# Performance work log

Hardware: AMD Instinct MI355X
Metric: run time of the kernel (lower is better)

The kernel has to match this reference:

```python
import jax, jax.numpy as jnp
import numpy as np

EMBED_DIM = 768
NUM_HEADS = 12
D_K = EMBED_DIM // NUM_HEADS
FFN_DIM = 3072
N_QUBITS = 8
LN_EPS = 1e-5


def layer_norm(x, g, b):
    mu = jnp.mean(x, axis=-1, keepdims=True)
    var = jnp.mean(jnp.square(x - mu), axis=-1, keepdims=True)
    return (x - mu) * jax.lax.rsqrt(var + LN_EPS) * g + b


def setup_inputs() -> dict:
    key = jax.random.key(0)
    ks = jax.random.split(key, 8)
    B, S = 4, 2048
    s_comb = 1.0 / np.sqrt(EMBED_DIM)
    s_w1 = 1.0 / np.sqrt(N_QUBITS)
    s_w2 = 1.0 / np.sqrt(FFN_DIM)
    return {
        "x": jax.random.normal(ks[0], (B, S, EMBED_DIM), jnp.float32),
        "combine_w": jax.random.uniform(ks[1], (EMBED_DIM, EMBED_DIM), jnp.float32, -s_comb, s_comb),
        "theta": jax.random.normal(ks[2], (N_QUBITS,), jnp.float32),
        "w1": jax.random.uniform(ks[3], (FFN_DIM, N_QUBITS), jnp.float32, -s_w1, s_w1),
        "w2": jax.random.uniform(ks[4], (EMBED_DIM, FFN_DIM), jnp.float32, -s_w2, s_w2),
        "ln1_g": jnp.ones((EMBED_DIM,), jnp.float32),
        "ln1_b": jnp.zeros((EMBED_DIM,), jnp.float32),
        "ln2_g": jnp.ones((EMBED_DIM,), jnp.float32),
        "ln2_b": jnp.zeros((EMBED_DIM,), jnp.float32),
    }


def reference(x, combine_w, theta, w1, w2, ln1_g, ln1_b, ln2_g, ln2_b):
    B, S, D = x.shape
    # --- attention (q = k = v = x split into heads; QLayer is never used in forward) ---
    xh = x.reshape(B, S, NUM_HEADS, D_K).transpose(0, 2, 1, 3)  # [B,H,S,dk]
    scores = jnp.einsum("bhqd,bhkd->bhqk", xh, xh) / jnp.sqrt(jnp.asarray(D_K, x.dtype))
    probs = jax.nn.softmax(scores, axis=-1)
    attn = jnp.einsum("bhqk,bhkd->bhqd", probs, xh)
    attn = attn.transpose(0, 2, 1, 3).reshape(B, S, D)
    attn_out = attn @ combine_w.T
    # --- residual + norm1 ---
    h = layer_norm(x + attn_out, ln1_g, ln1_b)
    # --- quantum FFN: RX(x_i) then RY(theta_i) per wire, <Z_i> = cos(x_i)*cos(theta_i) ---
    meas = jnp.cos(h[..., :N_QUBITS]) * jnp.cos(theta)  # [B,S,nq]
    ffn = jax.nn.relu(meas @ w1.T) @ w2.T               # [B,S,D]
    # --- residual + norm2 ---
    return layer_norm(h + ffn, ln2_g, ln2_b)
```

## Files before the change

### kernel.cpp

```cpp
#include <hip/hip_runtime.h>
#include <math.h>


#define B_    4
#define S_    2048
#define D_    768
#define H_    12
#define DK_   64
#define FFN_  3072
#define NQ_   8
#define M_    (B_ * S_)

typedef __attribute__((ext_vector_type(8))) short bf16x8;
typedef __attribute__((ext_vector_type(4))) float f32x4;

static __device__ __forceinline__ unsigned short f2bf(float f) {
    unsigned u = __float_as_uint(f);
    unsigned r = (u + 0x7FFFu + ((u >> 16) & 1u)) >> 16;
    return (unsigned short)r;
}
static __device__ __forceinline__ unsigned pk2(float a, float b) {
    return (unsigned)f2bf(a) | ((unsigned)f2bf(b) << 16);
}
static __device__ __forceinline__ bf16x8 pack8(float4 a, float4 b) {
    bf16x8 r;
    r[0] = (short)f2bf(a.x); r[1] = (short)f2bf(a.y);
    r[2] = (short)f2bf(a.z); r[3] = (short)f2bf(a.w);
    r[4] = (short)f2bf(b.x); r[5] = (short)f2bf(b.y);
    r[6] = (short)f2bf(b.z); r[7] = (short)f2bf(b.w);
    return r;
}

__global__ __launch_bounds__(256, 2)
void attn_mfma(const float* __restrict__ x, unsigned short* __restrict__ attnb)
{
    __shared__ __align__(16) short Ks[64 * 64];
    __shared__ __align__(16) short Vt[64 * 64];
    __shared__ __align__(16) short Ps[4 * 32 * 64];

    const int tid = threadIdx.x;
    const int w   = tid >> 6;
    const int l   = tid & 63;
    const int g   = l >> 4;
    const int l15 = l & 15;

    const int q0 = blockIdx.x * 128;
    const int hh = blockIdx.y;
    const int bb = blockIdx.z;

    const float* xh = x + ((size_t)bb * S_) * D_ + hh * DK_;

    bf16x8 qf[2][2];
    {
        const float* xq = xh + (size_t)(q0 + w * 32) * D_;
        #pragma unroll
        for (int qt = 0; qt < 2; ++qt)
            #pragma unroll
            for (int ks = 0; ks < 2; ++ks) {
                const float* p = xq + (size_t)(qt * 16 + l15) * D_ + ks * 32 + g * 8;
                float4 f0 = *reinterpret_cast<const float4*>(p);
                float4 f1 = *reinterpret_cast<const float4*>(p + 4);
                qf[qt][ks] = pack8(f0, f1);
            }
    }

    f32x4 oacc[2][4];
    float mrun[2][4], lrun[2][4];
    #pragma unroll
    for (int qt = 0; qt < 2; ++qt)
        #pragma unroll
        for (int i = 0; i < 4; ++i) {
            oacc[qt][i] = (f32x4){0.f, 0.f, 0.f, 0.f};
            mrun[qt][i] = -3.0e38f; lrun[qt][i] = 0.f;
        }

    short* Pw = Ps + w * 32 * 64;

    for (int kt = 0; kt < S_ / 64; ++kt) {
        __syncthreads();
        const float* xk = xh + (size_t)(kt * 64) * D_;

        #pragma unroll
        for (int it = 0; it < 2; ++it) {
            int c = tid + it * 256;
            int r = c >> 3, b = c & 7;
            const float* p = xk + (size_t)r * D_ + b * 8;
            float4 f0 = *reinterpret_cast<const float4*>(p);
            float4 f1 = *reinterpret_cast<const float4*>(p + 4);
            *reinterpret_cast<bf16x8*>(&Ks[r * 64 + ((b ^ (r & 7)) << 3)]) = pack8(f0, f1);
        }
        {
            int kv0 = (tid & 31) * 2;
            int dch = tid >> 5;
            unsigned* Vt32 = reinterpret_cast<unsigned*>(Vt);
            #pragma unroll
            for (int dp = 0; dp < 2; ++dp) {
                int d0 = dp * 32 + dch * 4;
                float4 fa = *reinterpret_cast<const float4*>(xk + (size_t)kv0 * D_ + d0);
                float4 fb = *reinterpret_cast<const float4*>(xk + (size_t)(kv0 + 1) * D_ + d0);
                const float* pa = reinterpret_cast<const float*>(&fa);
                const float* pb = reinterpret_cast<const float*>(&fb);
                #pragma unroll
                for (int j = 0; j < 4; ++j) {
                    int d = d0 + j;
                    Vt32[d * 32 + ((kv0 >> 1) ^ ((d & 7) << 2))] = pk2(pa[j], pb[j]);
                }
            }
        }
        __syncthreads();

        f32x4 sacc[2][4];
        #pragma unroll
        for (int qt = 0; qt < 2; ++qt)
            #pragma unroll
            for (int kj = 0; kj < 4; ++kj) sacc[qt][kj] = (f32x4){0.f, 0.f, 0.f, 0.f};

        #pragma unroll
        for (int ks = 0; ks < 2; ++ks) {
            bf16x8 kf[4];
            #pragma unroll
            for (int kj = 0; kj < 4; ++kj) {
                int r = kj * 16 + l15;
                kf[kj] = *reinterpret_cast<const bf16x8*>(
                    &Ks[r * 64 + (((ks * 4 + g) ^ (r & 7)) << 3)]);
            }
            #pragma unroll
            for (int qt = 0; qt < 2; ++qt)
                #pragma unroll
                for (int kj = 0; kj < 4; ++kj)
                    sacc[qt][kj] = __builtin_amdgcn_mfma_f32_16x16x32_bf16(
                        qf[qt][ks], kf[kj], sacc[qt][kj], 0, 0, 0);
        }

        #pragma unroll
        for (int qt = 0; qt < 2; ++qt) {
            #pragma unroll
            for (int reg = 0; reg < 4; ++reg) {
                float s0 = sacc[qt][0][reg] * 0.125f;
                float s1 = sacc[qt][1][reg] * 0.125f;
                float s2 = sacc[qt][2][reg] * 0.125f;
                float s3 = sacc[qt][3][reg] * 0.125f;
                float mx = fmaxf(fmaxf(s0, s1), fmaxf(s2, s3));
                #pragma unroll
                for (int msk = 1; msk < 16; msk <<= 1) mx = fmaxf(mx, __shfl_xor(mx, msk));
                float mnew = fmaxf(mrun[qt][reg], mx);
                float corr = __expf(mrun[qt][reg] - mnew);
                mrun[qt][reg] = mnew;
                float p0 = __expf(s0 - mnew), p1 = __expf(s1 - mnew);
                float p2 = __expf(s2 - mnew), p3 = __expf(s3 - mnew);
                float ps = (p0 + p1) + (p2 + p3);
                #pragma unroll
                for (int msk = 1; msk < 16; msk <<= 1) ps += __shfl_xor(ps, msk);
                lrun[qt][reg] = lrun[qt][reg] * corr + ps;
                #pragma unroll
                for (int dt = 0; dt < 4; ++dt) oacc[qt][dt][reg] *= corr;
                int q = qt * 16 + g * 4 + reg;
                short* pr = Pw + q * 64;
                int sw = (q & 7) << 3;
                pr[(0 * 16 + l15) ^ sw] = (short)f2bf(p0);
                pr[(1 * 16 + l15) ^ sw] = (short)f2bf(p1);
                pr[(2 * 16 + l15) ^ sw] = (short)f2bf(p2);
                pr[(3 * 16 + l15) ^ sw] = (short)f2bf(p3);
            }
        }

        #pragma unroll
        for (int ks = 0; ks < 2; ++ks) {
            bf16x8 pf[2], vf[4];
            #pragma unroll
            for (int qt = 0; qt < 2; ++qt) {
                int q = qt * 16 + l15;
                pf[qt] = *reinterpret_cast<const bf16x8*>(
                    &Pw[q * 64 + (((ks * 4 + g) ^ (q & 7)) << 3)]);
            }
            #pragma unroll
            for (int dt = 0; dt < 4; ++dt) {
                int d = dt * 16 + l15;
                vf[dt] = *reinterpret_cast<const bf16x8*>(
                    &Vt[d * 64 + (((ks * 4 + g) ^ (d & 7)) << 3)]);
            }
            #pragma unroll
            for (int qt = 0; qt < 2; ++qt)
                #pragma unroll
                for (int dt = 0; dt < 4; ++dt)
                    oacc[qt][dt] = __builtin_amdgcn_mfma_f32_16x16x32_bf16(
                        pf[qt], vf[dt], oacc[qt][dt], 0, 0, 0);
        }
    }

    unsigned short* ao = attnb + ((size_t)bb * S_ + q0 + w * 32) * D_ + hh * DK_;
    #pragma unroll
    for (int qt = 0; qt < 2; ++qt)
        #pragma unroll
        for (int reg = 0; reg < 4; ++reg) {
            int q = qt * 16 + g * 4 + reg;
            float inv = 1.0f / lrun[qt][reg];
            unsigned short* rp = ao + (size_t)q * D_;
            #pragma unroll
            for (int dt = 0; dt < 4; ++dt)
                rp[dt * 16 + l15] = f2bf(oacc[qt][dt][reg] * inv);
        }
}

__global__ __launch_bounds__(256, 2)
void gemm_combine(const unsigned short* __restrict__ A, const float* __restrict__ W,
                  const float* __restrict__ xres, float* __restrict__ y1)
{
    __shared__ __align__(16) short As[128 * 64];
    __shared__ __align__(16) short Bs[128 * 64];

    const int tid = threadIdx.x;
    const int w = tid >> 6, l = tid & 63, g = l >> 4, l15 = l & 15;
    const int wr = w >> 1, wc = w & 1;
    const int m0 = blockIdx.x * 128, n0 = blockIdx.y * 128;

    f32x4 acc[4][4];
    #pragma unroll
    for (int i = 0; i < 4; ++i)
        #pragma unroll
        for (int j = 0; j < 4; ++j) acc[i][j] = (f32x4){0.f, 0.f, 0.f, 0.f};

    for (int k0 = 0; k0 < D_; k0 += 64) {
        __syncthreads();
        #pragma unroll
        for (int it = 0; it < 4; ++it) {
            int c = tid + it * 256;
            int r = c >> 3, b = c & 7;
            bf16x8 v = *reinterpret_cast<const bf16x8*>(
                A + (size_t)(m0 + r) * D_ + k0 + b * 8);
            *reinterpret_cast<bf16x8*>(&As[r * 64 + ((b ^ (r & 7)) << 3)]) = v;
        }
        #pragma unroll
        for (int it = 0; it < 4; ++it) {
            int c = tid + it * 256;
            int r = c >> 3, b = c & 7;
            const float* p = W + (size_t)(n0 + r) * D_ + k0 + b * 8;
            float4 f0 = *reinterpret_cast<const float4*>(p);
            float4 f1 = *reinterpret_cast<const float4*>(p + 4);
            *reinterpret_cast<bf16x8*>(&Bs[r * 64 + ((b ^ (r & 7)) << 3)]) = pack8(f0, f1);
        }
        __syncthreads();

        #pragma unroll
        for (int ks = 0; ks < 2; ++ks) {
            bf16x8 af[4], bf[4];
            #pragma unroll
            for (int mt = 0; mt < 4; ++mt) {
                int r = wr * 64 + mt * 16 + l15;
                af[mt] = *reinterpret_cast<const bf16x8*>(
                    &As[r * 64 + (((ks * 4 + g) ^ (r & 7)) << 3)]);
            }
            #pragma unroll
            for (int nt = 0; nt < 4; ++nt) {
                int cc = wc * 64 + nt * 16 + l15;
                bf[nt] = *reinterpret_cast<const bf16x8*>(
                    &Bs[cc * 64 + (((ks * 4 + g) ^ (cc & 7)) << 3)]);
            }
            #pragma unroll
            for (int mt = 0; mt < 4; ++mt)
                #pragma unroll
                for (int nt = 0; nt < 4; ++nt)
                    acc[mt][nt] = __builtin_amdgcn_mfma_f32_16x16x32_bf16(
                        af[mt], bf[nt], acc[mt][nt], 0, 0, 0);
        }
    }

    #pragma unroll
    for (int mt = 0; mt < 4; ++mt)
        #pragma unroll
        for (int reg = 0; reg < 4; ++reg) {
            size_t row = (size_t)m0 + wr * 64 + mt * 16 + g * 4 + reg;
            #pragma unroll
            for (int nt = 0; nt < 4; ++nt) {
                int col = n0 + wc * 64 + nt * 16 + l15;
                y1[row * D_ + col] = acc[mt][nt][reg] + xres[row * D_ + col];
            }
        }
}

__global__ __launch_bounds__(256, 2)
void ffn_mfma(const float* __restrict__ hin, const float* __restrict__ theta,
              const float* __restrict__ w1, const float* __restrict__ w2,
              float* __restrict__ y2)
{
    __shared__ __align__(16) short Ts[128 * 64];
    __shared__ __align__(16) short Bs[128 * 64];
    __shared__ float meas_s[128][9];

    const int tid = threadIdx.x;
    const int w = tid >> 6, l = tid & 63, g = l >> 4, l15 = l & 15;
    const int wr = w >> 1, wc = w & 1;
    const int m0 = blockIdx.x * 128, n0 = blockIdx.y * 128;

    if (tid < 128) {
        const float* hp = hin + (size_t)(m0 + tid) * D_;
        #pragma unroll
        for (int q = 0; q < NQ_; ++q)
            meas_s[tid][q] = cosf(hp[q]) * cosf(theta[q]);
    }

    const int cp   = tid & 31;
    const int rblk = tid >> 5;
    unsigned* Ts32 = reinterpret_cast<unsigned*>(Ts);

    f32x4 acc[4][4];
    #pragma unroll
    for (int i = 0; i < 4; ++i)
        #pragma unroll
        for (int j = 0; j < 4; ++j) acc[i][j] = (f32x4){0.f, 0.f, 0.f, 0.f};

    for (int k0 = 0; k0 < FFN_; k0 += 64) {
        __syncthreads();
        #pragma unroll
        for (int it = 0; it < 4; ++it) {
            int c = tid + it * 256;
            int r = c >> 3, b = c & 7;
            const float* p = w2 + (size_t)(n0 + r) * FFN_ + k0 + b * 8;
            float4 f0 = *reinterpret_cast<const float4*>(p);
            float4 f1 = *reinterpret_cast<const float4*>(p + 4);
            *reinterpret_cast<bf16x8*>(&Bs[r * 64 + ((b ^ (r & 7)) << 3)]) = pack8(f0, f1);
        }
        {
            const float* wA = w1 + (size_t)(k0 + 2 * cp) * NQ_;
            const float* wB = wA + NQ_;
            float4 a0 = *reinterpret_cast<const float4*>(wA);
            float4 a1 = *reinterpret_cast<const float4*>(wA + 4);
            float4 b0 = *reinterpret_cast<const float4*>(wB);
            float4 b1 = *reinterpret_cast<const float4*>(wB + 4);
            const float* wAa = reinterpret_cast<const float*>(&a0);
            const float* wAb = reinterpret_cast<const float*>(&a1);
            const float* wBa = reinterpret_cast<const float*>(&b0);
            const float* wBb = reinterpret_cast<const float*>(&b1);
            #pragma unroll
            for (int i = 0; i < 16; ++i) {
                int r = rblk * 16 + i;
                float t0 = 0.f, t1 = 0.f;
                #pragma unroll
                for (int q = 0; q < 4; ++q) {
                    float m = meas_s[r][q];
                    t0 = fmaf(m, wAa[q], t0);
                    t1 = fmaf(m, wBa[q], t1);
                }
                #pragma unroll
                for (int q = 0; q < 4; ++q) {
                    float m = meas_s[r][q + 4];
                    t0 = fmaf(m, wAb[q], t0);
                    t1 = fmaf(m, wBb[q], t1);
                }
                t0 = fmaxf(t0, 0.f); t1 = fmaxf(t1, 0.f);
                Ts32[r * 32 + (cp ^ ((r & 7) << 2))] = pk2(t0, t1);
            }
        }
        __syncthreads();

        #pragma unroll
        for (int ks = 0; ks < 2; ++ks) {
            bf16x8 af[4], bf[4];
            #pragma unroll
            for (int mt = 0; mt < 4; ++mt) {
                int r = wr * 64 + mt * 16 + l15;
                af[mt] = *reinterpret_cast<const bf16x8*>(
                    &Ts[r * 64 + (((ks * 4 + g) ^ (r & 7)) << 3)]);
            }
            #pragma unroll
            for (int nt = 0; nt < 4; ++nt) {
                int cc = wc * 64 + nt * 16 + l15;
                bf[nt] = *reinterpret_cast<const bf16x8*>(
                    &Bs[cc * 64 + (((ks * 4 + g) ^ (cc & 7)) << 3)]);
            }
            #pragma unroll
            for (int mt = 0; mt < 4; ++mt)
                #pragma unroll
                for (int nt = 0; nt < 4; ++nt)
                    acc[mt][nt] = __builtin_amdgcn_mfma_f32_16x16x32_bf16(
                        af[mt], bf[nt], acc[mt][nt], 0, 0, 0);
        }
    }

    #pragma unroll
    for (int mt = 0; mt < 4; ++mt)
        #pragma unroll
        for (int reg = 0; reg < 4; ++reg) {
            size_t row = (size_t)m0 + wr * 64 + mt * 16 + g * 4 + reg;
            #pragma unroll
            for (int nt = 0; nt < 4; ++nt) {
                int col = n0 + wc * 64 + nt * 16 + l15;
                y2[row * D_ + col] = acc[mt][nt][reg] + hin[row * D_ + col];
            }
        }
}

__global__ __launch_bounds__(256, 4)
void ln_kernel(const float* __restrict__ in, const float* __restrict__ g,
               const float* __restrict__ bt, float* __restrict__ out)
{
    const int wave = threadIdx.x >> 6, lane = threadIdx.x & 63;
    const size_t row = (size_t)blockIdx.x * 4 + wave;
    const float* p = in + row * D_;
    float v[12];
    float sum = 0.f;
    #pragma unroll
    for (int c = 0; c < 3; ++c) {
        float4 f = *reinterpret_cast<const float4*>(p + (c * 64 + lane) * 4);
        v[c*4+0] = f.x; v[c*4+1] = f.y; v[c*4+2] = f.z; v[c*4+3] = f.w;
        sum += (f.x + f.y) + (f.z + f.w);
    }
    #pragma unroll
    for (int msk = 1; msk < 64; msk <<= 1) sum += __shfl_xor(sum, msk);
    const float mu = sum * (1.0f / 768.0f);
    float vs = 0.f;
    #pragma unroll
    for (int k = 0; k < 12; ++k) { float d = v[k] - mu; vs = fmaf(d, d, vs); }
    #pragma unroll
    for (int msk = 1; msk < 64; msk <<= 1) vs += __shfl_xor(vs, msk);
    const float rstd = rsqrtf(vs * (1.0f / 768.0f) + 1e-5f);
    float* po = out + row * D_;
    #pragma unroll
    for (int c = 0; c < 3; ++c) {
        const int base = (c * 64 + lane) * 4;
        float4 gg = *reinterpret_cast<const float4*>(g + base);
        float4 bb2 = *reinterpret_cast<const float4*>(bt + base);
        float4 r;
        r.x = (v[c*4+0] - mu) * rstd * gg.x + bb2.x;
        r.y = (v[c*4+1] - mu) * rstd * gg.y + bb2.y;
        r.z = (v[c*4+2] - mu) * rstd * gg.z + bb2.z;
        r.w = (v[c*4+3] - mu) * rstd * gg.w + bb2.w;
        *reinterpret_cast<float4*>(po + base) = r;
    }
}

extern "C" void kernel_launch(void* const* d_in, const int* in_sizes, int n_in,
                              void* d_out, int out_size, void* d_ws, size_t ws_size,
                              hipStream_t stream)
{
    const float* x   = (const float*)d_in[0];
    const float* cw  = (const float*)d_in[1];
    const float* th  = (const float*)d_in[2];
    const float* w1  = (const float*)d_in[3];
    const float* w2  = (const float*)d_in[4];
    const float* g1  = (const float*)d_in[5];
    const float* b1  = (const float*)d_in[6];
    const float* g2  = (const float*)d_in[7];
    const float* b2  = (const float*)d_in[8];
    float* out = (float*)d_out;

    const size_t NE = (size_t)M_ * D_;
    float* ws = (float*)d_ws;
    unsigned short* attnb = (unsigned short*)ws;
    float* hbuf = ws + NE;
    float* y1   = out;
    float* y2   = ws;

    attn_mfma   <<<dim3(S_ / 128, H_, B_), 256, 0, stream>>>(x, attnb);
    gemm_combine<<<dim3(M_ / 128, D_ / 128), 256, 0, stream>>>(attnb, cw, x, y1);
    ln_kernel   <<<dim3(M_ / 4), 256, 0, stream>>>(y1, g1, b1, hbuf);
    ffn_mfma    <<<dim3(M_ / 128, D_ / 128), 256, 0, stream>>>(hbuf, th, w1, w2, y2);
    ln_kernel   <<<dim3(M_ / 4), 256, 0, stream>>>(y2, g2, b2, out);
}
```

Before: 543.9 us.

## Pre-convert inputs to bf16, drop online softmax max, split FFN into T-build plus GEMM

A new first kernel converts x, combine_w and w2 to bf16 once. Attention then uses direct global-to-LDS loads into a double-buffered 128-key K tile, prefetches V in registers, and remaps the grid. Softmax drops the running max and rescaling: it uses plain exp2 and normalises by the row sum at the end, which can overflow for larger score magnitudes. The FFN now materialises the relu(meas·w1ᵀ) matrix in bf16 through a separate tbuild kernel and reuses a generic 64x128 bf16 GEMM for both projections. This trades a large extra HBM round trip for T against cheaper GEMM inner loops.

After: 541.2 us. No clear change (-0.5%).

```diff
diff --git a/kernel.cpp b/kernel.cpp
--- a/kernel.cpp
+++ b/kernel.cpp
@@ -11,6 +11,9 @@
 #define NQ_   8
 #define M_    (B_ * S_)
 
+#define AS1 __attribute__((address_space(1)))
+#define AS3 __attribute__((address_space(3)))
+
 typedef __attribute__((ext_vector_type(8))) short bf16x8;
 typedef __attribute__((ext_vector_type(4))) float f32x4;
 
@@ -19,8 +22,8 @@
     unsigned r = (u + 0x7FFFu + ((u >> 16) & 1u)) >> 16;
     return (unsigned short)r;
 }
-static __device__ __forceinline__ unsigned pk2(float a, float b) {
-    return (unsigned)f2bf(a) | ((unsigned)f2bf(b) << 16);
+static __device__ __forceinline__ float bf2f(unsigned short h) {
+    return __uint_as_float((unsigned)h << 16);
 }
 static __device__ __forceinline__ bf16x8 pack8(float4 a, float4 b) {
     bf16x8 r;
@@ -31,12 +34,30 @@
     return r;
 }
 
+#define XCH  786432
+#define CWCH 73728
+#define W2CH 294912
+__global__ void convert_all(const float* __restrict__ x, const float* __restrict__ cw,
+                            const float* __restrict__ w2,
+                            unsigned short* __restrict__ xb, unsigned short* __restrict__ cwb,
+                            unsigned short* __restrict__ w2b)
+{
+    int idx = blockIdx.x * 256 + threadIdx.x;
+    const float* src; unsigned short* dst; int c;
+    if (idx < XCH)              { src = x;  dst = xb;  c = idx; }
+    else if (idx < XCH + CWCH)  { src = cw; dst = cwb; c = idx - XCH; }
+    else { c = idx - XCH - CWCH; if (c >= W2CH) return; src = w2; dst = w2b; }
+    float4 f0 = *reinterpret_cast<const float4*>(src + (size_t)c * 8);
+    float4 f1 = *reinterpret_cast<const float4*>(src + (size_t)c * 8 + 4);
+    *reinterpret_cast<bf16x8*>(dst + (size_t)c * 8) = pack8(f0, f1);
+}
+
 __global__ __launch_bounds__(256, 2)
-void attn_mfma(const float* __restrict__ x, unsigned short* __restrict__ attnb)
-{
-    __shared__ __align__(16) short Ks[64 * 64];
-    __shared__ __align__(16) short Vt[64 * 64];
-    __shared__ __align__(16) short Ps[4 * 32 * 64];
+void attn_mfma(const unsigned short* __restrict__ xb, unsigned short* __restrict__ attnb)
+{
+    __shared__ __align__(16) short    Ks[2][128 * 64];
+    __shared__ __align__(16) unsigned Vt32[64 * 64];
+    __shared__ __align__(16) short    Ps[4][32 * 128];
 
     const int tid = threadIdx.x;
     const int w   = tid >> 6;
@@ -44,90 +65,103 @@
     const int g   = l >> 4;
     const int l15 = l & 15;
 
-    const int q0 = blockIdx.x * 128;
-    const int hh = blockIdx.y;
-    const int bb = blockIdx.z;
-
-    const float* xh = x + ((size_t)bb * S_) * D_ + hh * DK_;
+    const int flat = blockIdx.x;
+    const int rx = flat & 7;
+    const int t  = flat >> 3;
+    const int gq = t & 15;
+    const int G  = (t >> 4) * 8 + rx;
+    const int hh = G % 12, bb = G / 12;
+    const int q0 = gq * 128;
+
+    const unsigned short* xh = xb + ((size_t)bb * S_) * D_ + hh * DK_;
 
     bf16x8 qf[2][2];
     {
-        const float* xq = xh + (size_t)(q0 + w * 32) * D_;
+        const unsigned short* xq = xh + (size_t)(q0 + w * 32) * D_;
         #pragma unroll
         for (int qt = 0; qt < 2; ++qt)
             #pragma unroll
-            for (int ks = 0; ks < 2; ++ks) {
-                const float* p = xq + (size_t)(qt * 16 + l15) * D_ + ks * 32 + g * 8;
-                float4 f0 = *reinterpret_cast<const float4*>(p);
-                float4 f1 = *reinterpret_cast<const float4*>(p + 4);
-                qf[qt][ks] = pack8(f0, f1);
-            }
+            for (int ks = 0; ks < 2; ++ks)
+                qf[qt][ks] = *reinterpret_cast<const bf16x8*>(
+                    xq + (size_t)(qt * 16 + l15) * D_ + ks * 32 + g * 8);
     }
 
     f32x4 oacc[2][4];
-    float mrun[2][4], lrun[2][4];
+    float lsum[2][4];
     #pragma unroll
     for (int qt = 0; qt < 2; ++qt)
         #pragma unroll
         for (int i = 0; i < 4; ++i) {
             oacc[qt][i] = (f32x4){0.f, 0.f, 0.f, 0.f};
-            mrun[qt][i] = -3.0e38f; lrun[qt][i] = 0.f;
-        }
-
-    short* Pw = Ps + w * 32 * 64;
-
-    for (int kt = 0; kt < S_ / 64; ++kt) {
-        __syncthreads();
-        const float* xk = xh + (size_t)(kt * 64) * D_;
-
-        #pragma unroll
-        for (int it = 0; it < 2; ++it) {
+            lsum[qt][i] = 0.f;
+        }
+
+    short* Pw = Ps[w];
+    bf16x8 vh0, vh1, vh2, vh3;
+    const int kvp = tid & 63, dg = tid >> 6;
+
+    auto stageK = [&](int kt, int buf) {
+        const unsigned short* xk = xh + (size_t)(kt * 128) * D_;
+        #pragma unroll
+        for (int it = 0; it < 4; ++it) {
             int c = tid + it * 256;
-            int r = c >> 3, b = c & 7;
-            const float* p = xk + (size_t)r * D_ + b * 8;
-            float4 f0 = *reinterpret_cast<const float4*>(p);
-            float4 f1 = *reinterpret_cast<const float4*>(p + 4);
-            *reinterpret_cast<bf16x8*>(&Ks[r * 64 + ((b ^ (r & 7)) << 3)]) = pack8(f0, f1);
-        }
-        {
-            int kv0 = (tid & 31) * 2;
-            int dch = tid >> 5;
-            unsigned* Vt32 = reinterpret_cast<unsigned*>(Vt);
-            #pragma unroll
-            for (int dp = 0; dp < 2; ++dp) {
-                int d0 = dp * 32 + dch * 4;
-                float4 fa = *reinterpret_cast<const float4*>(xk + (size_t)kv0 * D_ + d0);
-                float4 fb = *reinterpret_cast<const float4*>(xk + (size_t)(kv0 + 1) * D_ + d0);
-                const float* pa = reinterpret_cast<const float*>(&fa);
-                const float* pb = reinterpret_cast<const float*>(&fb);
-                #pragma unroll
-                for (int j = 0; j < 4; ++j) {
-                    int d = d0 + j;
-                    Vt32[d * 32 + ((kv0 >> 1) ^ ((d & 7) << 2))] = pk2(pa[j], pb[j]);
-                }
-            }
-        }
-        __syncthreads();
-
-        f32x4 sacc[2][4];
+            int r = c >> 3, b2 = c & 7;
+            const unsigned short* gsrc = xk + (size_t)r * D_ + ((b2 ^ (r & 7)) << 3);
+            __builtin_amdgcn_global_load_lds(
+                (const AS1 void*)gsrc,
+                (AS3 void*)(&Ks[buf][0] + ((it * 256 + w * 64) << 3)), 16, 0, 0);
+        }
+    };
+    auto loadV = [&](int kt) {
+        const unsigned short* ra = xh + (size_t)(kt * 128 + 2 * kvp) * D_ + dg * 16;
+        vh0 = *reinterpret_cast<const bf16x8*>(ra);
+        vh1 = *reinterpret_cast<const bf16x8*>(ra + 8);
+        vh2 = *reinterpret_cast<const bf16x8*>(ra + D_);
+        vh3 = *reinterpret_cast<const bf16x8*>(ra + D_ + 8);
+    };
+    auto writeV = [&]() {
+        #pragma unroll
+        for (int j = 0; j < 8; ++j) {
+            int d0 = dg * 16 + j;
+            Vt32[d0 * 64 + (kvp ^ ((d0 & 7) << 2))] =
+                (unsigned)(unsigned short)vh0[j] | ((unsigned)(unsigned short)vh2[j] << 16);
+            int d1 = dg * 16 + 8 + j;
+            Vt32[d1 * 64 + (kvp ^ ((d1 & 7) << 2))] =
+                (unsigned)(unsigned short)vh1[j] | ((unsigned)(unsigned short)vh3[j] << 16);
+        }
+    };
+
+    stageK(0, 0);
+    loadV(0);
+    writeV();
+    __syncthreads();
+
+    for (int kt = 0; kt < S_ / 128; ++kt) {
+        const int cur = kt & 1;
+        if (kt < S_ / 128 - 1) {
+            stageK(kt + 1, cur ^ 1);
+            loadV(kt + 1);
+        }
+
+        f32x4 sacc[2][8];
         #pragma unroll
         for (int qt = 0; qt < 2; ++qt)
             #pragma unroll
-            for (int kj = 0; kj < 4; ++kj) sacc[qt][kj] = (f32x4){0.f, 0.f, 0.f, 0.f};
+            for (int kj = 0; kj < 8; ++kj) sacc[qt][kj] = (f32x4){0.f, 0.f, 0.f, 0.f};
 
         #pragma unroll
         for (int ks = 0; ks < 2; ++ks) {
-            bf16x8 kf[4];
-            #pragma unroll
-            for (int kj = 0; kj < 4; ++kj) {
+            bf16x8 kf[8];
+            #pragma unroll
+            for (int kj = 0; kj < 8; ++kj) {
                 int r = kj * 16 + l15;
                 kf[kj] = *reinterpret_cast<const bf16x8*>(
-                    &Ks[r * 64 + (((ks * 4 + g) ^ (r & 7)) << 3)]);
+                    &Ks[cur][r * 64 + (((ks * 4 + g) ^ (r & 7)) << 3)]);
             }
             #pragma unroll
             for (int qt = 0; qt < 2; ++qt)
                 #pragma unroll
-                for (int kj = 0; kj < 4; ++kj)
+                for (int kj = 0; kj < 8; ++kj)
                     sacc[qt][kj] = __builtin_amdgcn_mfma_f32_16x16x32_bf16(
                         qf[qt][ks], kf[kj], sacc[qt][kj], 0, 0, 0);
         }
@@ -136,48 +170,36 @@
         for (int qt = 0; qt < 2; ++qt) {
             #pragma unroll
             for (int reg = 0; reg < 4; ++reg) {
-                float s0 = sacc[qt][0][reg] * 0.125f;
-                float s1 = sacc[qt][1][reg] * 0.125f;
-                float s2 = sacc[qt][2][reg] * 0.125f;
-                float s3 = sacc[qt][3][reg] * 0.125f;
-                float mx = fmaxf(fmaxf(s0, s1), fmaxf(s2, s3));
+                int q = qt * 16 + g * 4 + reg;
+                short* pr = Pw + q * 128;
+                int qs = q & 7;
+                float psum = 0.f;
                 #pragma unroll
-                for (int msk = 1; msk < 16; msk <<= 1) mx = fmaxf(mx, __shfl_xor(mx, msk));
-                float mnew = fmaxf(mrun[qt][reg], mx);
-                float corr = __expf(mrun[qt][reg] - mnew);
-                mrun[qt][reg] = mnew;
-                float p0 = __expf(s0 - mnew), p1 = __expf(s1 - mnew);
-                float p2 = __expf(s2 - mnew), p3 = __expf(s3 - mnew);
-                float ps = (p0 + p1) + (p2 + p3);
-                #pragma unroll
-                for (int msk = 1; msk < 16; msk <<= 1) ps += __shfl_xor(ps, msk);
-                lrun[qt][reg] = lrun[qt][reg] * corr + ps;
-                #pragma unroll
-                for (int dt = 0; dt < 4; ++dt) oacc[qt][dt][reg] *= corr;
-                int q = qt * 16 + g * 4 + reg;
-                short* pr = Pw + q * 64;
-                int sw = (q & 7) << 3;
-                pr[(0 * 16 + l15) ^ sw] = (short)f2bf(p0);
-                pr[(1 * 16 + l15) ^ sw] = (short)f2bf(p1);
-                pr[(2 * 16 + l15) ^ sw] = (short)f2bf(p2);
-                pr[(3 * 16 + l15) ^ sw] = (short)f2bf(p3);
-            }
-        }
-
-        #pragma unroll
-        for (int ks = 0; ks < 2; ++ks) {
+                for (int kj = 0; kj < 8; ++kj) {
+                    float p = exp2f(sacc[qt][kj][reg] * 0.18033688f);
+                    psum += p;
+                    int c = kj * 16 + l15;
+                    pr[(((c >> 3) ^ qs) << 3) | (c & 7)] =
+                        (short)((__float_as_uint(p) + 0x8000u) >> 16);
+                }
+                lsum[qt][reg] += psum;
+            }
+        }
+
+        #pragma unroll
+        for (int ks = 0; ks < 4; ++ks) {
             bf16x8 pf[2], vf[4];
             #pragma unroll
             for (int qt = 0; qt < 2; ++qt) {
                 int q = qt * 16 + l15;
                 pf[qt] = *reinterpret_cast<const bf16x8*>(
-                    &Pw[q * 64 + (((ks * 4 + g) ^ (q & 7)) << 3)]);
+                    &Pw[q * 128 + (((ks * 4 + g) ^ (q & 7)) << 3)]);
             }
             #pragma unroll
             for (int dt = 0; dt < 4; ++dt) {
                 int d = dt * 16 + l15;
                 vf[dt] = *reinterpret_cast<const bf16x8*>(
-                    &Vt[d * 64 + (((ks * 4 + g) ^ (d & 7)) << 3)]);
+                    &Vt32[d * 64 + ((ks * 16 + g * 4) ^ ((d & 7) << 2))]);
             }
             #pragma unroll
             for (int qt = 0; qt < 2; ++qt)
@@ -186,6 +208,10 @@
                     oacc[qt][dt] = __builtin_amdgcn_mfma_f32_16x16x32_bf16(
                         pf[qt], vf[dt], oacc[qt][dt], 0, 0, 0);
         }
+
+        __syncthreads();
+        if (kt < S_ / 128 - 1) writeV();
+        __syncthreads();
     }
 
     unsigned short* ao = attnb + ((size_t)bb * S_ + q0 + w * 32) * D_ + hh * DK_;
@@ -193,8 +219,11 @@
     for (int qt = 0; qt < 2; ++qt)
         #pragma unroll
         for (int reg = 0; reg < 4; ++reg) {
+            float s = lsum[qt][reg];
+            s += __shfl_xor(s, 1); s += __shfl_xor(s, 2);
+            s += __shfl_xor(s, 4); s += __shfl_xor(s, 8);
+            float inv = 1.0f / s;
             int q = qt * 16 + g * 4 + reg;
-            float inv = 1.0f / lrun[qt][reg];
             unsigned short* rp = ao + (size_t)q * D_;
             #pragma unroll
             for (int dt = 0; dt < 4; ++dt)
@@ -202,51 +231,51 @@
         }
 }
 
-__global__ __launch_bounds__(256, 2)
-void gemm_combine(const unsigned short* __restrict__ A, const float* __restrict__ W,
-                  const float* __restrict__ xres, float* __restrict__ y1)
-{
-    __shared__ __align__(16) short As[128 * 64];
+template<int KDIM>
+__global__ __launch_bounds__(256, 3)
+void gemm_bf16(const unsigned short* __restrict__ A, const unsigned short* __restrict__ Bw,
+               const float* __restrict__ res, float* __restrict__ out)
+{
+    __shared__ __align__(16) short As[64 * 64];
     __shared__ __align__(16) short Bs[128 * 64];
 
     const int tid = threadIdx.x;
     const int w = tid >> 6, l = tid & 63, g = l >> 4, l15 = l & 15;
     const int wr = w >> 1, wc = w & 1;
-    const int m0 = blockIdx.x * 128, n0 = blockIdx.y * 128;
-
-    f32x4 acc[4][4];
-    #pragma unroll
-    for (int i = 0; i < 4; ++i)
+    const int m0 = blockIdx.x * 64, n0 = blockIdx.y * 128;
+
+    f32x4 acc[2][4];
+    #pragma unroll
+    for (int i = 0; i < 2; ++i)
         #pragma unroll
         for (int j = 0; j < 4; ++j) acc[i][j] = (f32x4){0.f, 0.f, 0.f, 0.f};
 
-    for (int k0 = 0; k0 < D_; k0 += 64) {
+    for (int k0 = 0; k0 < KDIM; k0 += 64) {
         __syncthreads();
+        #pragma unroll
+        for (int it = 0; it < 2; ++it) {
+            int c = tid + it * 256;
+            int r = c >> 3, b = c & 7;
+            const unsigned short* ga = A + (size_t)(m0 + r) * KDIM + k0 + ((b ^ (r & 7)) << 3);
+            __builtin_amdgcn_global_load_lds((const AS1 void*)ga,
+                (AS3 void*)(As + ((it * 256 + w * 64) << 3)), 16, 0, 0);
+        }
         #pragma unroll
         for (int it = 0; it < 4; ++it) {
             int c = tid + it * 256;
             int r = c >> 3, b = c & 7;
-            bf16x8 v = *reinterpret_cast<const bf16x8*>(
-                A + (size_t)(m0 + r) * D_ + k0 + b * 8);
-            *reinterpret_cast<bf16x8*>(&As[r * 64 + ((b ^ (r & 7)) << 3)]) = v;
-        }
-        #pragma unroll
-        for (int it = 0; it < 4; ++it) {
-            int c = tid + it * 256;
-            int r = c >> 3, b = c & 7;
-            const float* p = W + (size_t)(n0 + r) * D_ + k0 + b * 8;
-            float4 f0 = *reinterpret_cast<const float4*>(p);
-            float4 f1 = *reinterpret_cast<const float4*>(p + 4);
-            *reinterpret_cast<bf16x8*>(&Bs[r * 64 + ((b ^ (r & 7)) << 3)]) = pack8(f0, f1);
+            const unsigned short* gb = Bw + (size_t)(n0 + r) * KDIM + k0 + ((b ^ (r & 7)) << 3);
+            __builtin_amdgcn_global_load_lds((const AS1 void*)gb,
+                (AS3 void*)(Bs + ((it * 256 + w * 64) << 3)), 16, 0, 0);
         }
         __syncthreads();
 
         #pragma unroll
         for (int ks = 0; ks < 2; ++ks) {
-            bf16x8 af[4], bf[4];
-            #pragma unroll
-            for (int mt = 0; mt < 4; ++mt) {
-                int r = wr * 64 + mt * 16 + l15;
+            bf16x8 af[2], bf[4];
+            #pragma unroll
+            for (int mt = 0; mt < 2; ++mt) {
+                int r = wr * 32 + mt * 16 + l15;
                 af[mt] = *reinterpret_cast<const bf16x8*>(
                     &As[r * 64 + (((ks * 4 + g) ^ (r & 7)) << 3)]);
             }
@@ -257,7 +286,7 @@
                     &Bs[cc * 64 + (((ks * 4 + g) ^ (cc & 7)) << 3)]);
             }
             #pragma unroll
-            for (int mt = 0; mt < 4; ++mt)
+            for (int mt = 0; mt < 2; ++mt)
                 #pragma unroll
                 for (int nt = 0; nt < 4; ++nt)
                     acc[mt][nt] = __builtin_amdgcn_mfma_f32_16x16x32_bf16(
@@ -266,128 +295,65 @@
     }
 
     #pragma unroll
-    for (int mt = 0; mt < 4; ++mt)
+    for (int mt = 0; mt < 2; ++mt)
         #pragma unroll
         for (int reg = 0; reg < 4; ++reg) {
-            size_t row = (size_t)m0 + wr * 64 + mt * 16 + g * 4 + reg;
+            size_t row = (size_t)m0 + wr * 32 + mt * 16 + g * 4 + reg;
             #pragma unroll
             for (int nt = 0; nt < 4; ++nt) {
                 int col = n0 + wc * 64 + nt * 16 + l15;
-                y1[row * D_ + col] = acc[mt][nt][reg] + xres[row * D_ + col];
+                out[row * D_ + col] = acc[mt][nt][reg] + res[row * D_ + col];
             }
         }
 }
 
 __global__ __launch_bounds__(256, 2)
-void ffn_mfma(const float* __restrict__ hin, const float* __restrict__ theta,
-              const float* __restrict__ w1, const float* __restrict__ w2,
-              float* __restrict__ y2)
-{
-    __shared__ __align__(16) short Ts[128 * 64];
-    __shared__ __align__(16) short Bs[128 * 64];
-    __shared__ float meas_s[128][9];
+void tbuild(const float* __restrict__ h, const float* __restrict__ theta,
+            const float* __restrict__ w1, unsigned short* __restrict__ Tb)
+{
+    __shared__ __align__(16) short w1s[FFN_ * NQ_];
 
     const int tid = threadIdx.x;
-    const int w = tid >> 6, l = tid & 63, g = l >> 4, l15 = l & 15;
-    const int wr = w >> 1, wc = w & 1;
-    const int m0 = blockIdx.x * 128, n0 = blockIdx.y * 128;
-
-    if (tid < 128) {
-        const float* hp = hin + (size_t)(m0 + tid) * D_;
-        #pragma unroll
-        for (int q = 0; q < NQ_; ++q)
-            meas_s[tid][q] = cosf(hp[q]) * cosf(theta[q]);
-    }
-
-    const int cp   = tid & 31;
-    const int rblk = tid >> 5;
-    unsigned* Ts32 = reinterpret_cast<unsigned*>(Ts);
-
-    f32x4 acc[4][4];
-    #pragma unroll
-    for (int i = 0; i < 4; ++i)
-        #pragma unroll
-        for (int j = 0; j < 4; ++j) acc[i][j] = (f32x4){0.f, 0.f, 0.f, 0.f};
-
-    for (int k0 = 0; k0 < FFN_; k0 += 64) {
-        __syncthreads();
-        #pragma unroll
-        for (int it = 0; it < 4; ++it) {
-            int c = tid + it * 256;
-            int r = c >> 3, b = c & 7;
-            const float* p = w2 + (size_t)(n0 + r) * FFN_ + k0 + b * 8;
-            float4 f0 = *reinterpret_cast<const float4*>(p);
-            float4 f1 = *reinterpret_cast<const float4*>(p + 4);
-            *reinterpret_cast<bf16x8*>(&Bs[r * 64 + ((b ^ (r & 7)) << 3)]) = pack8(f0, f1);
-        }
-        {
-            const float* wA = w1 + (size_t)(k0 + 2 * cp) * NQ_;
-            const float* wB = wA + NQ_;
-            float4 a0 = *reinterpret_cast<const float4*>(wA);
-            float4 a1 = *reinterpret_cast<const float4*>(wA + 4);
-            float4 b0 = *reinterpret_cast<const float4*>(wB);
-            float4 b1 = *reinterpret_cast<const float4*>(wB + 4);
-            const float* wAa = reinterpret_cast<const float*>(&a0);
-            const float* wAb = reinterpret_cast<const float*>(&a1);
-            const float* wBa = reinterpret_cast<const float*>(&b0);
-            const float* wBb = reinterpret_cast<const float*>(&b1);
-            #pragma unroll
-            for (int i = 0; i < 16; ++i) {
-                int r = rblk * 16 + i;
-                float t0 = 0.f, t1 = 0.f;
+    const int w = tid >> 6, l = tid & 63;
+
+    #pragma unroll
+    for (int it = 0; it < 12; ++it) {
+        int c = tid + it * 256;
+        float4 f0 = *reinterpret_cast<const float4*>(w1 + (size_t)c * 8);
+        float4 f1 = *reinterpret_cast<const float4*>(w1 + (size_t)c * 8 + 4);
+        *reinterpret_cast<bf16x8*>(&w1s[(c ^ ((c >> 3) & 7)) * 8]) = pack8(f0, f1);
+    }
+    __syncthreads();
+
+    float cth[NQ_];
+    #pragma unroll
+    for (int q = 0; q < NQ_; ++q) cth[q] = cosf(theta[q]);
+
+    #pragma unroll
+    for (int rr = 0; rr < 4; ++rr) {
+        int row = blockIdx.x * 16 + w * 4 + rr;
+        const float* hp = h + (size_t)row * D_;
+        float meas[NQ_];
+        #pragma unroll
+        for (int q = 0; q < NQ_; ++q) meas[q] = cosf(hp[q]) * cth[q];
+        unsigned short* outp = Tb + (size_t)row * FFN_;
+        #pragma unroll
+        for (int itc = 0; itc < 6; ++itc) {
+            int cbase = itc * 512 + l * 8;
+            bf16x8 tv;
+            #pragma unroll
+            for (int cc = 0; cc < 8; ++cc) {
+                bf16x8 wv = *reinterpret_cast<const bf16x8*>(
+                    &w1s[((cbase + cc) ^ (l & 7)) * 8]);
+                float t = 0.f;
                 #pragma unroll
-                for (int q = 0; q < 4; ++q) {
-                    float m = meas_s[r][q];
-                    t0 = fmaf(m, wAa[q], t0);
-                    t1 = fmaf(m, wBa[q], t1);
-                }
-                #pragma unroll
-                for (int q = 0; q < 4; ++q) {
-                    float m = meas_s[r][q + 4];
-                    t0 = fmaf(m, wAb[q], t0);
-                    t1 = fmaf(m, wBb[q], t1);
-                }
-                t0 = fmaxf(t0, 0.f); t1 = fmaxf(t1, 0.f);
-                Ts32[r * 32 + (cp ^ ((r & 7) << 2))] = pk2(t0, t1);
-            }
-        }
-        __syncthreads();
-
-        #pragma unroll
-        for (int ks = 0; ks < 2; ++ks) {
-            bf16x8 af[4], bf[4];
-            #pragma unroll
-            for (int mt = 0; mt < 4; ++mt) {
-                int r = wr * 64 + mt * 16 + l15;
-                af[mt] = *reinterpret_cast<const bf16x8*>(
-                    &Ts[r * 64 + (((ks * 4 + g) ^ (r & 7)) << 3)]);
-            }
-            #pragma unroll
-            for (int nt = 0; nt < 4; ++nt) {
-                int cc = wc * 64 + nt * 16 + l15;
-                bf[nt] = *reinterpret_cast<const bf16x8*>(
-                    &Bs[cc * 64 + (((ks * 4 + g) ^ (cc & 7)) << 3)]);
-            }
-            #pragma unroll
-            for (int mt = 0; mt < 4; ++mt)
-                #pragma unroll
-                for (int nt = 0; nt < 4; ++nt)
-                    acc[mt][nt] = __builtin_amdgcn_mfma_f32_16x16x32_bf16(
-                        af[mt], bf[nt], acc[mt][nt], 0, 0, 0);
-        }
-    }
-
-    #pragma unroll
-    for (int mt = 0; mt < 4; ++mt)
-        #pragma unroll
-        for (int reg = 0; reg < 4; ++reg) {
-            size_t row = (size_t)m0 + wr * 64 + mt * 16 + g * 4 + reg;
-            #pragma unroll
-            for (int nt = 0; nt < 4; ++nt) {
-                int col = n0 + wc * 64 + nt * 16 + l15;
-                y2[row * D_ + col] = acc[mt][nt][reg] + hin[row * D_ + col];
-            }
-        }
+                for (int q = 0; q < NQ_; ++q)
+                    t = fmaf(meas[q], bf2f((unsigned short)wv[q]), t);
+                tv[cc] = (short)f2bf(fmaxf(t, 0.f));
+            }
+            *reinterpret_cast<bf16x8*>(&outp[cbase]) = tv;
+        }
+    }
 }
 
 __global__ __launch_bounds__(256, 4)
@@ -444,16 +410,23 @@
     const float* b2  = (const float*)d_in[8];
     float* out = (float*)d_out;
 
-    const size_t NE = (size_t)M_ * D_;
-    float* ws = (float*)d_ws;
-    unsigned short* attnb = (unsigned short*)ws;
-    float* hbuf = ws + NE;
-    float* y1   = out;
-    float* y2   = ws;
-
-    attn_mfma   <<<dim3(S_ / 128, H_, B_), 256, 0, stream>>>(x, attnb);
-    gemm_combine<<<dim3(M_ / 128, D_ / 128), 256, 0, stream>>>(attnb, cw, x, y1);
-    ln_kernel   <<<dim3(M_ / 4), 256, 0, stream>>>(y1, g1, b1, hbuf);
-    ffn_mfma    <<<dim3(M_ / 128, D_ / 128), 256, 0, stream>>>(hbuf, th, w1, w2, y2);
-    ln_kernel   <<<dim3(M_ / 4), 256, 0, stream>>>(y2, g2, b2, out);
-}
+    const size_t HB  = 25165824;
+    const size_t TBB = 50331648;
+    const size_t CWB = 1179648;
+
+    char* wsc = (char*)d_ws;
+    unsigned short* xbuf  = (unsigned short*)wsc;
+    float*          hbuf  = (float*)wsc;
+    unsigned short* attnb = (unsigned short*)(wsc + HB);
+    unsigned short* Tb    = (unsigned short*)(wsc + HB);
+    unsigned short* cwb   = (unsigned short*)(wsc + HB + TBB);
+    unsigned short* w2b   = (unsigned short*)(wsc + HB + TBB + CWB);
+
+    convert_all    <<<dim3((XCH + CWCH + W2CH) / 256), 256, 0, stream>>>(x, cw, w2, xbuf, cwb, w2b);
+    attn_mfma      <<<dim3(16 * H_ * B_), 256, 0, stream>>>(xbuf, attnb);
+    gemm_bf16<D_>  <<<dim3(M_ / 64, D_ / 128), 256, 0, stream>>>(attnb, cwb, x, out);
+    ln_kernel      <<<dim3(M_ / 4), 256, 0, stream>>>(out, g1, b1, hbuf);
+    tbuild         <<<dim3(M_ / 16), 256, 0, stream>>>(hbuf, th, w1, Tb);
+    gemm_bf16<FFN_><<<dim3(M_ / 64, D_ / 128), 256, 0, stream>>>(Tb, w2b, hbuf, out);
+    ln_kernel      <<<dim3(M_ / 4), 256, 0, stream>>>(out, g2, b2, out);
+}
```
